# Kernel optimization log

Measured on AMD Instinct MI355X. Metric: run time of the kernel, lower is better.

Reference implementation:

```python
import jax, jax.numpy as jnp
import numpy as np

N_HEAD = 8


def build_mask(T, N):
    """Boolean mask [L, L], True = blocked. Mirrors the torch st_mask construction
    for text_mask_mode='part_only', text_to_motion_attn=False, all domains present."""
    L = 3 * T + 5 * N
    motion = 3 * T
    m = np.zeros((L, L), dtype=bool)
    # motion x motion: start fully blocked, then carve block-causal structure
    m[:motion, :motion] = True
    causal = np.tril(np.ones((T, T), dtype=bool))          # incl. diagonal
    strict = np.tril(np.ones((T, T), dtype=bool), k=-1)    # strictly lower
    m[0:T, 0:T] = ~causal
    m[T:2*T, 0:T] = ~causal
    m[T:2*T, T:2*T] = ~strict
    m[T:2*T, 2*T:3*T] = ~strict
    m[2*T:3*T, 0:T] = ~causal
    m[2*T:3*T, T:2*T] = ~causal
    m[2*T:3*T, 2*T:3*T] = ~strict
    # motion queries cannot see text keys
    m[:motion, motion:] = True
    # text queries cannot see motion keys (text_to_motion_attn=False)
    m[motion:, :motion] = True
    # part_only: upper-body rows see upper/torso/whole/simple_tag text domains;
    # lower-body rows see lower/torso/whole/simple_tag text domains
    ts = motion
    up, down = slice(T, 2*T), slice(2*T, 3*T)
    for d in (0, 2, 3, 4):
        m[up, ts + d*N: ts + (d+1)*N] = False
    for d in (1, 2, 3, 4):
        m[down, ts + d*N: ts + (d+1)*N] = False
    # text x text region stays all-False (full attention among text tokens)
    return jnp.asarray(m)


def setup_inputs() -> dict:
    key = jax.random.key(0)
    ks = jax.random.split(key, 9)
    B, T_motion, N, C = 2, 1024, 64, 512
    L = 3 * T_motion + 5 * N
    s = 1.0 / np.sqrt(C)
    return {
        "x": jax.random.normal(ks[0], (B, L, C), dtype=jnp.float32),
        "Wq": jax.random.normal(ks[1], (C, C), dtype=jnp.float32) * s,
        "bq": jnp.zeros((C,), dtype=jnp.float32),
        "Wk": jax.random.normal(ks[2], (C, C), dtype=jnp.float32) * s,
        "bk": jnp.zeros((C,), dtype=jnp.float32),
        "Wv": jax.random.normal(ks[3], (C, C), dtype=jnp.float32) * s,
        "bv": jnp.zeros((C,), dtype=jnp.float32),
        "Wp": jax.random.normal(ks[4], (C, C), dtype=jnp.float32) * s,
        "bp": jnp.zeros((C,), dtype=jnp.float32),
        "T_motion": T_motion,
        "N": N,
    }


def reference(x, Wq, bq, Wk, bk, Wv, bv, Wp, bp, T_motion, N):
    B, L, C = x.shape
    H = N_HEAD
    dh = C // H
    mask = build_mask(int(T_motion), int(N))  # [L, L] bool, True = blocked

    def split_heads(t):  # [B, L, C] -> [B, H, L, dh]
        return t.reshape(B, L, H, dh).transpose(0, 2, 1, 3)

    q = split_heads(x @ Wq + bq)
    k = split_heads(x @ Wk + bk)
    v = split_heads(x @ Wv + bv)

    att = jnp.einsum("bhqd,bhkd->bhqk", q, k) * (1.0 / np.sqrt(dh))
    att = jnp.where(mask[None, None], -jnp.inf, att)
    att = jax.nn.softmax(att, axis=-1)
    y = jnp.einsum("bhqk,bhkd->bhqd", att, v)
    y = y.transpose(0, 2, 1, 3).reshape(B, L, C)
    return y @ Wp + bp
```

## Files before the change

### kernel.cpp

```cpp
#include <hip/hip_runtime.h>
#include <hip/hip_bf16.h>
#include <math.h>

typedef __attribute__((ext_vector_type(8))) short bf16x8;
typedef __attribute__((ext_vector_type(4))) short short4v;
typedef __attribute__((ext_vector_type(4))) float f32x4;
typedef __attribute__((ext_vector_type(2))) unsigned int u32x2;

#define DEVI __device__ __forceinline__

constexpr int Bb  = 2;
constexpr int Tm  = 1024;
constexpr int Ntx = 64;
constexpr int Hh  = 8;
constexpr int Ll  = 3*Tm + 5*Ntx;
constexpr int Mm  = Bb*Ll;
constexpr int MOT = 3*Tm;
constexpr int UPH = 75;
constexpr int PST = 72;

DEVI short f2b(float f) {
  unsigned u = __builtin_bit_cast(unsigned, f);
  u = u + 0x7fffu + ((u >> 16) & 1u);
  return (short)(u >> 16);
}

DEVI void gld16(const void* g, void* l) {
  __builtin_amdgcn_global_load_lds(
      (const __attribute__((address_space(1))) unsigned*)g,
      (__attribute__((address_space(3))) unsigned*)l, 16, 0, 0);
}

DEVI f32x4 mfma16(bf16x8 a, bf16x8 b, f32x4 c) {
  return __builtin_amdgcn_mfma_f32_16x16x32_bf16(a, b, c, 0, 0, 0);
}


__global__ __launch_bounds__(256) void prep_kern(
    const float* __restrict__ x,  short* __restrict__ xb,
    const float* __restrict__ Wq, const float* __restrict__ Wk,
    const float* __restrict__ Wv, const float* __restrict__ Wp,
    short* __restrict__ WtQKV, short* __restrict__ WpT) {
  if (blockIdx.x < 3392) {
    int i = (blockIdx.x*256 + threadIdx.x)*4;
    float4 v = *(const float4*)(x + i);
    short4v r;
    r.x = f2b(v.x); r.y = f2b(v.y); r.z = f2b(v.z); r.w = f2b(v.w);
    *(short4v*)(xb + i) = r;
  } else {
    int idx = (blockIdx.x - 3392)*256 + threadIdx.x;
    int mat = idx >> 18;
    int n = (idx >> 9) & 511;
    int k = idx & 511;
    const float* W = (mat == 0) ? Wq : (mat == 1) ? Wk : (mat == 2) ? Wv : Wp;
    short s = f2b(W[k*512 + n]);
    if (mat < 3) WtQKV[((size_t)(mat*512 + n))*512 + k] = s;
    else         WpT[(size_t)n*512 + k] = s;
  }
}


template<int MODE>
__global__ __launch_bounds__(256) void gemm_bt(
    const short* __restrict__ A, const short* __restrict__ Bt,
    const float* __restrict__ bias_q, const float* __restrict__ bias_k,
    const float* __restrict__ bias_v,
    short* __restrict__ Qb, short* __restrict__ Kb, short* __restrict__ Vt,
    float* __restrict__ outf) {
  __shared__ __align__(16) short At[128*32];
  __shared__ __align__(16) short Bs[128*32];
  const int tid = threadIdx.x;
  const int w = tid >> 6, lane = tid & 63;
  const int col = lane & 15, g = lane >> 4;
  const int tm = blockIdx.x, tn = blockIdx.y;
  const int wm = w >> 1, wn = w & 1;

  f32x4 acc[4][4] = {};

  for (int k0 = 0; k0 < 512; k0 += 32) {
    __syncthreads();
#pragma unroll
    for (int it = 0; it < 2; ++it) {
      int e0 = w*512 + it*2048 + lane*8;
      int row = e0 >> 5, cc = e0 & 31;
      gld16(A  + (size_t)(tm*128 + row)*512 + k0 + cc, At + w*512 + it*2048);
      gld16(Bt + (size_t)(tn*128 + row)*512 + k0 + cc, Bs + w*512 + it*2048);
    }
    __syncthreads();
    bf16x8 af[4], bfr[4];
#pragma unroll
    for (int i = 0; i < 4; ++i)
      af[i] = *(const bf16x8*)(At + (wm*64 + i*16 + col)*32 + g*8);
#pragma unroll
    for (int j = 0; j < 4; ++j)
      bfr[j] = *(const bf16x8*)(Bs + (wn*64 + j*16 + col)*32 + g*8);
#pragma unroll
    for (int i = 0; i < 4; ++i)
#pragma unroll
      for (int j = 0; j < 4; ++j)
        acc[i][j] = mfma16(af[i], bfr[j], acc[i][j]);
  }

#pragma unroll
  for (int i = 0; i < 4; ++i) {
    int mbase = tm*128 + wm*64 + i*16 + g*4;
#pragma unroll
    for (int j = 0; j < 4; ++j) {
      int ncol = tn*128 + wn*64 + j*16 + col;
#pragma unroll
      for (int r = 0; r < 4; ++r) {
        int mrow = mbase + r;
        float v = acc[i][j][r];
        if constexpr (MODE == 0) {
          float bias = (ncol < 512) ? bias_q[ncol]
                     : (ncol < 1024) ? bias_k[ncol - 512] : bias_v[ncol - 1024];
          v += bias;
          int bb = (mrow >= Ll) ? 1 : 0;
          int lpos = mrow - bb*Ll;
          int nn = ncol & 511;
          int h = nn >> 6, dd = nn & 63;
          int bh = bb*8 + h;
          if (ncol < 512) {
            Qb[((size_t)(bh*Ll + lpos))*64 + dd] = f2b(v*0.18033688f);
          } else if (ncol < 1024) {
            Kb[((size_t)(bh*Ll + lpos))*64 + dd] = f2b(v);
          } else {
            Vt[((size_t)(bh*64 + dd))*Ll + lpos] = f2b(v);
          }
        } else {
          outf[(size_t)mrow*512 + ncol] = v + bias_q[ncol];
        }
      }
    }
  }
}


__global__ __launch_bounds__(256) void attn_kern(
    const short* __restrict__ Qb, const short* __restrict__ Kb,
    const short* __restrict__ Vt, float* __restrict__ slots,
    short* __restrict__ attout) {
  __shared__ __align__(16) short Kls[2][4096];
  __shared__ __align__(16) short Vls[2][4096];
  __shared__ __align__(16) short Pls[4][32*PST];
  const int tid = threadIdx.x;
  const int w = tid >> 6, lane = tid & 63;
  const int col = lane & 15, g = lane >> 4;

  const int v  = (blockIdx.x & 7)*150 + (blockIdx.x >> 3);
  const int bh = v / UPH;
  const int lr = v - bh*UPH;

  int qsec, seg = 0, j = 0, t3 = 0;
  if (lr < 56) {
    int jj = lr/7, s = lr - jj*7;
    j = 7 - jj;
    if (s == 0)      qsec = 0;
    else if (s <= 3) { qsec = 1; seg = s - 1; }
    else             { qsec = 2; seg = s - 4; }
  } else if (lr < 72) {
    int t = lr - 56; qsec = 1 + (t & 1); j = t >> 1; seg = 3;
  } else { qsec = 3; t3 = lr - 72; }

  const int q0b = (qsec < 3) ? qsec*Tm + j*128 : MOT + ((t3 == 2) ? 192 : t3*128);
  const int t0w = j*128 + w*32;
  const int q0w = q0b + w*32;

  int kbase = 0, off = 0, nb;
  bool masked;
  if (qsec == 3)      { kbase = MOT;  nb = 5;       masked = false; }
  else if (qsec == 0) { kbase = 0;    nb = 2*j + 2; masked = true; off = 0; }
  else if (seg == 0)  { kbase = 0;    nb = 2*j + 2; masked = true; off = 0; }
  else if (seg == 1)  { kbase = Tm;   nb = 2*j + 2; masked = true; off = (qsec == 1) ? 1 : 0; }
  else if (seg == 2)  { kbase = 2*Tm; nb = 2*j + 2; masked = true; off = 1; }
  else                { kbase = 0;    nb = 4;       masked = false; }

  auto keyof = [&](int i) -> int {
    if (qsec == 3) return MOT + i*64;
    if (!masked) { int d = (i == 0) ? ((qsec == 1) ? 0 : 1) : i + 1; return MOT + d*64; }
    return kbase + i*64;
  };

  const short* Kbase_ = Kb + (size_t)bh*Ll*64;
  const short* Vbase_ = Vt + (size_t)bh*64*Ll;

  bf16x8 aq[2][2];
#pragma unroll
  for (int qf = 0; qf < 2; ++qf) {
    const short* p = Qb + ((size_t)bh*Ll + q0w + qf*16 + col)*64;
    aq[qf][0] = *(const bf16x8*)(p + g*8);
    aq[qf][1] = *(const bf16x8*)(p + 32 + g*8);
  }
  const int qv[2] = { t0w + col, t0w + 16 + col };

  float ls[2] = {0.f, 0.f};
  f32x4 out[2][4] = {};

  auto stage = [&](int buf, int key0) {
#pragma unroll
    for (int it = 0; it < 2; ++it) {
      int L = it*4096 + tid*16;
      int row = L >> 7;
      int sw = (row & 7) << 4;
      gld16((const char*)Kbase_ + (size_t)key0*128 + (L ^ sw),
            (char*)&Kls[buf][0] + it*4096 + w*1024);
      gld16((const char*)(Vbase_ + (size_t)row*Ll + key0) + ((L & 127) ^ sw),
            (char*)&Vls[buf][0] + it*4096 + w*1024);
    }
  };

  auto compute = [&](int buf, int i) {
    const int swc = (col & 7) << 4;
    f32x4 s[2][4];
    __builtin_amdgcn_s_setprio(1);
#pragma unroll
    for (int kk = 0; kk < 4; ++kk) {
      const char* base = (const char*)&Kls[buf][0] + (kk*16 + col)*128;
      bf16x8 k0 = *(const bf16x8*)(base + ((g*16) ^ swc));
      bf16x8 k1 = *(const bf16x8*)(base + ((64 + g*16) ^ swc));
#pragma unroll
      for (int qf = 0; qf < 2; ++qf) {
        f32x4 t = {0,0,0,0};
        t = mfma16(k0, aq[qf][0], t);
        t = mfma16(k1, aq[qf][1], t);
        s[qf][kk] = t;
      }
    }
    __builtin_amdgcn_s_setprio(0);
    const bool dm = masked && (i*64 + 63 + off > t0w);
    const int kl = i*64 + off + g*4;
    short* pw = &Pls[w][0];
#pragma unroll
    for (int qf = 0; qf < 2; ++qf) {
      float lsl = 0.f;
#pragma unroll
      for (int kk = 0; kk < 4; ++kk) {
        float pe[4];
#pragma unroll
        for (int r = 0; r < 4; ++r) {
          float p = __builtin_amdgcn_exp2f(s[qf][kk][r]);
          if (dm && (kl + kk*16 + r > qv[qf])) p = 0.f;
          pe[r] = p; lsl += p;
        }
        unsigned pk0, pk1;
        asm("v_cvt_pk_bf16_f32 %0, %1, %2" : "=v"(pk0) : "v"(pe[0]), "v"(pe[1]));
        asm("v_cvt_pk_bf16_f32 %0, %1, %2" : "=v"(pk1) : "v"(pe[2]), "v"(pe[3]));
        u32x2 pk; pk.x = pk0; pk.y = pk1;
        *(u32x2*)(pw + (qf*16 + col)*PST + kk*16 + g*4) = pk;
      }
      ls[qf] += lsl;
    }
    bf16x8 pa[2][2];
#pragma unroll
    for (int qf = 0; qf < 2; ++qf) {
      const short* base2 = &Pls[w][0] + (qf*16 + col)*PST;
      pa[qf][0] = *(const bf16x8*)(base2 + g*8);
      pa[qf][1] = *(const bf16x8*)(base2 + 32 + g*8);
    }
    __builtin_amdgcn_s_setprio(1);
#pragma unroll
    for (int ch = 0; ch < 4; ++ch) {
      const char* base = (const char*)&Vls[buf][0] + (ch*16 + col)*128;
      bf16x8 v0 = *(const bf16x8*)(base + ((g*16) ^ swc));
      bf16x8 v1 = *(const bf16x8*)(base + ((64 + g*16) ^ swc));
#pragma unroll
      for (int qf = 0; qf < 2; ++qf) {
        out[qf][ch] = mfma16(pa[qf][0], v0, out[qf][ch]);
        out[qf][ch] = mfma16(pa[qf][1], v1, out[qf][ch]);
      }
    }
    __builtin_amdgcn_s_setprio(0);
  };

  stage(0, keyof(0));
  for (int i = 0; i < nb; ++i) {
    if (i + 1 < nb) {
      stage((i + 1) & 1, keyof(i + 1));
      asm volatile("s_waitcnt vmcnt(4)" ::: "memory");
    } else {
      asm volatile("s_waitcnt vmcnt(0)" ::: "memory");
    }
    __builtin_amdgcn_sched_barrier(0);
    __builtin_amdgcn_s_barrier();
    bool skip = masked && (t0w + 31 < i*64 + off);
    if (!skip) compute(i & 1, i);
    __builtin_amdgcn_s_barrier();
  }

  float rs[2];
#pragma unroll
  for (int qf = 0; qf < 2; ++qf) {
    float t = ls[qf];
    t += __shfl_xor(t, 16);
    t += __shfl_xor(t, 32);
    rs[qf] = t;
  }

  if (qsec == 1 || qsec == 2) {
    float* sp = slots + ((((size_t)bh*2 + (qsec - 1))*8 + j)*4 + seg)*8320;
#pragma unroll
    for (int qf = 0; qf < 2; ++qf) {
#pragma unroll
      for (int ch = 0; ch < 4; ++ch)
#pragma unroll
        for (int r = 0; r < 4; ++r)
          sp[(w*32 + qf*16 + g*4 + r)*64 + ch*16 + col] = out[qf][ch][r];
      if (g == 0)
        sp[8192 + w*32 + qf*16 + col] = rs[qf];
    }
  } else {
    const int b = bh >> 3, h = bh & 7;
#pragma unroll
    for (int qf = 0; qf < 2; ++qf)
#pragma unroll
      for (int r = 0; r < 4; ++r) {
        float dv = __shfl(rs[qf], g*4 + r);
        float inv = 1.0f / dv;
        size_t rowoff = ((size_t)(b*Ll + q0w + qf*16 + g*4 + r))*512 + h*64;
#pragma unroll
        for (int ch = 0; ch < 4; ++ch)
          attout[rowoff + ch*16 + col] = f2b(out[qf][ch][r]*inv);
      }
  }
}

__global__ __launch_bounds__(256) void fin_kern(const float* __restrict__ slots,
                                                short* __restrict__ attout) {
  const int w = threadIdx.x >> 6, lane = threadIdx.x & 63;
  const int ridx = blockIdx.x*4 + w;
  const int bh = ridx >> 11;
  const int rr = ridx & 2047;
  const int qsec = 1 + (rr >> 10);
  const int rl = rr & 1023;
  const int j = rl >> 7;
  const int row_local = rl & 127;
  const float* base = slots + (((size_t)bh*2 + (qsec - 1))*8 + j)*4*8320;
  float a = 0.f, l = 0.f;
#pragma unroll
  for (int s = 0; s < 4; ++s) {
    a += base[s*8320 + row_local*64 + lane];
    l += base[s*8320 + 8192 + row_local];
  }
  const int b = bh >> 3, h = bh & 7;
  attout[((size_t)(b*Ll + qsec*Tm + rl))*512 + h*64 + lane] = f2b(a / l);
}


extern "C" void kernel_launch(void* const* d_in, const int* in_sizes, int n_in,
                              void* d_out, int out_size, void* d_ws, size_t ws_size,
                              hipStream_t stream) {
  const float* x  = (const float*)d_in[0];
  const float* Wq = (const float*)d_in[1];
  const float* bq = (const float*)d_in[2];
  const float* Wk = (const float*)d_in[3];
  const float* bk = (const float*)d_in[4];
  const float* Wv = (const float*)d_in[5];
  const float* bv = (const float*)d_in[6];
  const float* Wp = (const float*)d_in[7];
  const float* bp = (const float*)d_in[8];
  float* out = (float*)d_out;

  short* ws = (short*)d_ws;
  constexpr size_t SZ  = (size_t)Mm*512;
  short* xb    = ws;
  short* WtQKV = xb + SZ;
  short* WpT   = WtQKV + (size_t)1536*512;
  short* Qb    = WpT + (size_t)512*512;
  short* Kb    = Qb + SZ;
  short* Vt    = Kb + SZ;
  short* att   = Vt + SZ;
  float* slots = (float*)(att + SZ);

  prep_kern<<<dim3(3392 + 4096), dim3(256), 0, stream>>>(x, xb, Wq, Wk, Wv, Wp,
                                                         WtQKV, WpT);
  gemm_bt<0><<<dim3(53, 12), dim3(256), 0, stream>>>(xb, WtQKV, bq, bk, bv,
                                                     Qb, Kb, Vt, nullptr);
  attn_kern<<<dim3(1200), dim3(256), 0, stream>>>(Qb, Kb, Vt, slots, att);
  fin_kern<<<dim3(8192), dim3(256), 0, stream>>>(slots, att);
  gemm_bt<1><<<dim3(53, 4), dim3(256), 0, stream>>>(att, WpT, bp, nullptr, nullptr,
                                                    nullptr, nullptr, nullptr, out);
}
```

Measured before the change: 97.29 us.

## Fuse split-K combine into attention via atomic last-block reduction

Removes the separate fin_kern launch. Each split-segment attention block now writes its partial output and row sum, then bumps a per-chunk atomic counter. The last of the four segments to arrive sums the partials and writes the normalized bf16 output. Counters are zeroed by an extra block in prep_kern. This saves a kernel launch and the pass that re-reads the slots, at the cost of a fence, an atomic and a serialized tail reduction in the winning blocks.

Measured after the change: 264.4 us. +171.8%, slower.

```diff
diff --git a/kernel.cpp b/kernel.cpp
--- a/kernel.cpp
+++ b/kernel.cpp
@@ -40,14 +40,14 @@
     const float* __restrict__ x,  short* __restrict__ xb,
     const float* __restrict__ Wq, const float* __restrict__ Wk,
     const float* __restrict__ Wv, const float* __restrict__ Wp,
-    short* __restrict__ WtQKV, short* __restrict__ WpT) {
+    short* __restrict__ WtQKV, short* __restrict__ WpT, int* __restrict__ cnt) {
   if (blockIdx.x < 3392) {
     int i = (blockIdx.x*256 + threadIdx.x)*4;
     float4 v = *(const float4*)(x + i);
     short4v r;
     r.x = f2b(v.x); r.y = f2b(v.y); r.z = f2b(v.z); r.w = f2b(v.w);
     *(short4v*)(xb + i) = r;
-  } else {
+  } else if (blockIdx.x < 3392 + 4096) {
     int idx = (blockIdx.x - 3392)*256 + threadIdx.x;
     int mat = idx >> 18;
     int n = (idx >> 9) & 511;
@@ -56,6 +56,8 @@
     short s = f2b(W[k*512 + n]);
     if (mat < 3) WtQKV[((size_t)(mat*512 + n))*512 + k] = s;
     else         WpT[(size_t)n*512 + k] = s;
+  } else {
+    cnt[threadIdx.x] = 0;
   }
 }
 
@@ -139,10 +141,11 @@
 __global__ __launch_bounds__(256) void attn_kern(
     const short* __restrict__ Qb, const short* __restrict__ Kb,
     const short* __restrict__ Vt, float* __restrict__ slots,
-    short* __restrict__ attout) {
+    int* __restrict__ cnt, short* __restrict__ attout) {
   __shared__ __align__(16) short Kls[2][4096];
   __shared__ __align__(16) short Vls[2][4096];
   __shared__ __align__(16) short Pls[4][32*PST];
+  __shared__ int winflag;
   const int tid = threadIdx.x;
   const int w = tid >> 6, lane = tid & 63;
   const int col = lane & 15, g = lane >> 4;
@@ -296,8 +299,10 @@
     rs[qf] = t;
   }
 
+  const int b = bh >> 3, h = bh & 7;
   if (qsec == 1 || qsec == 2) {
-    float* sp = slots + ((((size_t)bh*2 + (qsec - 1))*8 + j)*4 + seg)*8320;
+    const int cidx = (bh*2 + (qsec - 1))*8 + j;
+    float* sp = slots + ((size_t)cidx*4 + seg)*8320;
 #pragma unroll
     for (int qf = 0; qf < 2; ++qf) {
 #pragma unroll
@@ -308,8 +313,31 @@
       if (g == 0)
         sp[8192 + w*32 + qf*16 + col] = rs[qf];
     }
+    __threadfence();
+    if (tid == 0) {
+      int old = __hip_atomic_fetch_add(cnt + cidx, 1, __ATOMIC_ACQ_REL,
+                                       __HIP_MEMORY_SCOPE_AGENT);
+      winflag = (old == 3);
+    }
+    __syncthreads();
+    if (winflag) {
+      const float* base4 = slots + (size_t)cidx*4*8320;
+#pragma unroll 4
+      for (int rl2 = 0; rl2 < 32; ++rl2) {
+        int row_local = w*32 + rl2;
+        float a = 0.f, l = 0.f;
+#pragma unroll
+        for (int s2 = 0; s2 < 4; ++s2) {
+          a += __hip_atomic_load(base4 + s2*8320 + row_local*64 + lane,
+                                 __ATOMIC_RELAXED, __HIP_MEMORY_SCOPE_AGENT);
+          l += __hip_atomic_load(base4 + s2*8320 + 8192 + row_local,
+                                 __ATOMIC_RELAXED, __HIP_MEMORY_SCOPE_AGENT);
+        }
+        int row = qsec*Tm + j*128 + row_local;
+        attout[((size_t)(b*Ll + row))*512 + h*64 + lane] = f2b(a / l);
+      }
+    }
   } else {
-    const int b = bh >> 3, h = bh & 7;
 #pragma unroll
     for (int qf = 0; qf < 2; ++qf)
 #pragma unroll
@@ -322,27 +350,6 @@
           attout[rowoff + ch*16 + col] = f2b(out[qf][ch][r]*inv);
       }
   }
-}
-
-__global__ __launch_bounds__(256) void fin_kern(const float* __restrict__ slots,
-                                                short* __restrict__ attout) {
-  const int w = threadIdx.x >> 6, lane = threadIdx.x & 63;
-  const int ridx = blockIdx.x*4 + w;
-  const int bh = ridx >> 11;
-  const int rr = ridx & 2047;
-  const int qsec = 1 + (rr >> 10);
-  const int rl = rr & 1023;
-  const int j = rl >> 7;
-  const int row_local = rl & 127;
-  const float* base = slots + (((size_t)bh*2 + (qsec - 1))*8 + j)*4*8320;
-  float a = 0.f, l = 0.f;
-#pragma unroll
-  for (int s = 0; s < 4; ++s) {
-    a += base[s*8320 + row_local*64 + lane];
-    l += base[s*8320 + 8192 + row_local];
-  }
-  const int b = bh >> 3, h = bh & 7;
-  attout[((size_t)(b*Ll + qsec*Tm + rl))*512 + h*64 + lane] = f2b(a / l);
 }
 
 
@@ -370,13 +377,13 @@
   short* Vt    = Kb + SZ;
   short* att   = Vt + SZ;
   float* slots = (float*)(att + SZ);
-
-  prep_kern<<<dim3(3392 + 4096), dim3(256), 0, stream>>>(x, xb, Wq, Wk, Wv, Wp,
-                                                         WtQKV, WpT);
+  int*   cnt   = (int*)(slots + (size_t)256*4*8320);
+
+  prep_kern<<<dim3(3392 + 4096 + 1), dim3(256), 0, stream>>>(x, xb, Wq, Wk, Wv, Wp,
+                                                             WtQKV, WpT, cnt);
   gemm_bt<0><<<dim3(53, 12), dim3(256), 0, stream>>>(xb, WtQKV, bq, bk, bv,
                                                      Qb, Kb, Vt, nullptr);
-  attn_kern<<<dim3(1200), dim3(256), 0, stream>>>(Qb, Kb, Vt, slots, att);
-  fin_kern<<<dim3(8192), dim3(256), 0, stream>>>(slots, att);
+  attn_kern<<<dim3(1200), dim3(256), 0, stream>>>(Qb, Kb, Vt, slots, cnt, att);
   gemm_bt<1><<<dim3(53, 4), dim3(256), 0, stream>>>(att, WpT, bp, nullptr, nullptr,
                                                     nullptr, nullptr, nullptr, out);
 }
```
